# Kernel tuning notes

Measured on AMD Instinct MI355X. Metric: run time of the kernel, lower is better.

## Reference

```python
import jax, jax.numpy as jnp
import numpy as np

B, N, D, H = 32, 512, 768, 12
HD = D // H  # 64
EPS = 1e-5


def layer_norm(x, g, b):
    mu = jnp.mean(x, axis=-1, keepdims=True)
    var = jnp.mean((x - mu) ** 2, axis=-1, keepdims=True)
    return (x - mu) / jnp.sqrt(var + EPS) * g + b


def setup_inputs() -> dict:
    key = jax.random.key(0)
    ks = jax.random.split(key, 10)
    x = jax.random.normal(ks[0], (B, N, D), dtype=jnp.float32)
    adj = jax.random.randint(ks[1], (B, N, N), 0, 2).astype(jnp.int32)
    adj = jnp.maximum(adj, jnp.eye(N, dtype=jnp.int32)[None])  # self-loops
    init = lambda k, shape: (jax.random.normal(k, shape, dtype=jnp.float32) * 0.02)
    return {
        "x": x, "adj": adj,
        "wq": init(ks[2], (D, D)), "bq": jnp.zeros((D,), jnp.float32),
        "wk": init(ks[3], (D, D)), "bk": jnp.zeros((D,), jnp.float32),
        "wv": init(ks[4], (D, D)), "bv": jnp.zeros((D,), jnp.float32),
        "wo": init(ks[5], (D, D)), "bo": jnp.zeros((D,), jnp.float32),
        "g1": jnp.ones((D,), jnp.float32), "b1": jnp.zeros((D,), jnp.float32),
        "g2": jnp.ones((D,), jnp.float32), "b2": jnp.zeros((D,), jnp.float32),
        "w_ffn1": init(ks[6], (D, 4 * D)), "b_ffn1": jnp.zeros((4 * D,), jnp.float32),
        "w_ffn2": init(ks[7], (4 * D, D)), "b_ffn2": jnp.zeros((D,), jnp.float32),
    }


def reference(x, adj, wq, bq, wk, bk, wv, bv, wo, bo, g1, b1, g2, b2,
              w_ffn1, b_ffn1, w_ffn2, b_ffn2):
    scale = HD ** -0.5
    h = layer_norm(x, g1, b1)
    split = lambda t: t.reshape(B, N, H, HD).transpose(0, 2, 1, 3)  # [B,H,N,HD]
    q = split(h @ wq + bq)
    k = split(h @ wk + bk)
    v = split(h @ wv + bv)
    scores = jnp.einsum('bhnd,bhmd->bhnm', q, k) * scale  # [B,H,N,N]
    scores = jnp.where(adj[:, None, :, :] == 0, -jnp.inf, scores)
    attn = jax.nn.softmax(scores, axis=-1)
    attn = jnp.nan_to_num(attn, nan=0.0)  # rows with no edges -> 0
    out = jnp.einsum('bhnm,bhmd->bhnd', attn, v)
    out = out.transpose(0, 2, 1, 3).reshape(B, N, D)
    out = out @ wo + bo + x  # residual (dropout=0, eval mode)
    h2 = layer_norm(out, g2, b2)
    ffn = jax.nn.gelu(h2 @ w_ffn1 + b_ffn1, approximate=False) @ w_ffn2 + b_ffn2
    return out + ffn
```

## Files before the change

kernel.cpp:

```cpp
#include <hip/hip_runtime.h>


#define Bn 32
#define Nn 512
#define Dn 768
#define Hn 12
#define HDn 64
#define Mn (Bn * Nn)
#define DFn 3072
#define MCHUNK 8192

typedef unsigned short u16;
typedef unsigned long long u64;
typedef short bf16x8 __attribute__((ext_vector_type(8)));
typedef float f32x4 __attribute__((ext_vector_type(4)));
typedef unsigned short u16x8 __attribute__((ext_vector_type(8)));

__device__ __forceinline__ float b2f(u16 u) {
    return __uint_as_float(((unsigned int)u) << 16);
}
__device__ __forceinline__ u16 f2b(float f) {
    unsigned int u = __float_as_uint(f);
    u += 0x7fffu + ((u >> 16) & 1u);
    return (u16)(u >> 16);
}
__device__ __forceinline__ float loadDyn(const void* p, size_t i, int f) {
    return f ? ((const float*)p)[i] : b2f(((const u16*)p)[i]);
}
__device__ __forceinline__ float gelu_exact(float x) {
    return 0.5f * x * (1.0f + erff(x * 0.70710678118654752f));
}

__device__ __forceinline__ void gl_lds16(const u16* g, u16* l) {
    __builtin_amdgcn_global_load_lds(
        (const __attribute__((address_space(1))) void*)(unsigned long long)(const void*)g,
        (__attribute__((address_space(3))) void*)(unsigned)(unsigned long long)(void*)l,
        16, 0, 0);
}

__global__ __launch_bounds__(256) void sniff_k(const u16* __restrict__ x,
                                               int* __restrict__ flag) {
    const int idx = blockIdx.x * 256 + threadIdx.x;
    u16x8 a = *(const u16x8*)&x[(size_t)idx * 8];
    int cnt = 0;
#pragma unroll
    for (int e = 0; e < 8; e++)
        cnt += ((a[e] & 0x7F80) == 0x7F80) ? 1 : 0;
#pragma unroll
    for (int off = 1; off <= 32; off <<= 1) cnt += __shfl_xor(cnt, off, 64);
    if ((threadIdx.x & 63) == 0 && cnt > 0) atomicAdd(flag, cnt);
}

__device__ __forceinline__ int flagval(const int* flagp) {
    return (*flagp > 32) ? 1 : 0;
}

__global__ __launch_bounds__(256) void pack_bias_k(
    const void* __restrict__ bq, const void* __restrict__ bk,
    const void* __restrict__ bv, const void* __restrict__ bo,
    const void* __restrict__ bf1, const void* __restrict__ bf2,
    float* __restrict__ out, const int* __restrict__ flagp) {
    const int f = flagval(flagp);
    const int i = blockIdx.x * 256 + threadIdx.x;
    if (i >= 6912) return;
    const void* src;
    int off;
    if (i < 768)       { src = bq;  off = i; }
    else if (i < 1536) { src = bk;  off = i - 768; }
    else if (i < 2304) { src = bv;  off = i - 1536; }
    else if (i < 3072) { src = bo;  off = i - 2304; }
    else if (i < 6144) { src = bf1; off = i - 3072; }
    else               { src = bf2; off = i - 6144; }
    out[i] = loadDyn(src, off, f);
}

__global__ __launch_bounds__(256) void mask_build_k(
    const int* __restrict__ adj, u64* __restrict__ mask) {
    const int idx = blockIdx.x * 256 + threadIdx.x;
    const size_t base = (size_t)(idx >> 3) * Nn + (size_t)(idx & 7) * 64;
    const int4* p = (const int4*)(adj + base);
    u64 m = 0;
#pragma unroll
    for (int c = 0; c < 16; c++) {
        int4 a = p[c];
        if (a.x) m |= 1ull << (c * 4 + 0);
        if (a.y) m |= 1ull << (c * 4 + 1);
        if (a.z) m |= 1ull << (c * 4 + 2);
        if (a.w) m |= 1ull << (c * 4 + 3);
    }
    mask[idx] = m;
}

__global__ __launch_bounds__(256) void transpose_k(
    const void* __restrict__ in, u16* __restrict__ out, int R, int C,
    const int* __restrict__ flagp) {
    const int f = flagval(flagp);
    __shared__ u16 tile[32][33];
    int c0 = blockIdx.x * 32, r0 = blockIdx.y * 32;
    int tx = threadIdx.x, ty = threadIdx.y;
#pragma unroll
    for (int i = 0; i < 32; i += 8)
        tile[ty + i][tx] = f2b(loadDyn(in, (size_t)(r0 + ty + i) * C + c0 + tx, f));
    __syncthreads();
#pragma unroll
    for (int i = 0; i < 32; i += 8)
        out[(size_t)(c0 + ty + i) * R + r0 + tx] = tile[tx][ty + i];
}

__global__ __launch_bounds__(256) void vtrans_k(
    const u16* __restrict__ v, u16* __restrict__ vt) {
    __shared__ u16 tile[32][33];
    const int bh = blockIdx.z;
    const int d0 = blockIdx.x * 32;
    const int n0 = blockIdx.y * 32;
    const int b = bh / Hn, h = bh % Hn;
    const int tx = threadIdx.x, ty = threadIdx.y;
#pragma unroll
    for (int i = 0; i < 32; i += 8)
        tile[ty + i][tx] =
            v[(size_t)(b * Nn + n0 + ty + i) * Dn + h * HDn + d0 + tx];
    __syncthreads();
#pragma unroll
    for (int i = 0; i < 32; i += 8)
        vt[((size_t)bh * HDn + d0 + ty + i) * Nn + n0 + tx] = tile[tx][ty + i];
}

template <int XDYN>
__global__ __launch_bounds__(256) void ln_k(
    const void* __restrict__ x, const void* __restrict__ g,
    const void* __restrict__ b, u16* __restrict__ y,
    const int* __restrict__ flagp) {
    const int f = flagval(flagp);
    const int t = threadIdx.x;
    const int row = blockIdx.x * 8 + (t >> 5);
    const int l32 = t & 31;
    const size_t base = (size_t)row * Dn;
    float v[24];
    if (XDYN == 0 || f == 0) {
        const u16* xp = (const u16*)x;
#pragma unroll
        for (int kk = 0; kk < 3; kk++) {
            u16x8 a = *(const u16x8*)&xp[base + kk * 256 + l32 * 8];
#pragma unroll
            for (int e = 0; e < 8; e++) v[kk * 8 + e] = b2f(a[e]);
        }
    } else {
#pragma unroll
        for (int kk = 0; kk < 3; kk++)
#pragma unroll
            for (int e = 0; e < 8; e++)
                v[kk * 8 + e] = loadDyn(x, base + kk * 256 + l32 * 8 + e, f);
    }
    float s = 0.f;
#pragma unroll
    for (int i = 0; i < 24; i++) s += v[i];
#pragma unroll
    for (int off = 1; off <= 16; off <<= 1) s += __shfl_xor(s, off, 64);
    const float mu = s * (1.0f / Dn);
    float d2 = 0.f;
#pragma unroll
    for (int i = 0; i < 24; i++) { float d = v[i] - mu; d2 += d * d; }
#pragma unroll
    for (int off = 1; off <= 16; off <<= 1) d2 += __shfl_xor(d2, off, 64);
    const float rstd = rsqrtf(d2 * (1.0f / Dn) + 1e-5f);
#pragma unroll
    for (int kk = 0; kk < 3; kk++) {
        const int c0 = kk * 256 + l32 * 8;
        u16x8 o;
        if (f == 0) {
            u16x8 gv = *(const u16x8*)&((const u16*)g)[c0];
            u16x8 bv = *(const u16x8*)&((const u16*)b)[c0];
#pragma unroll
            for (int e = 0; e < 8; e++)
                o[e] = f2b((v[kk * 8 + e] - mu) * rstd * b2f(gv[e]) + b2f(bv[e]));
        } else {
#pragma unroll
            for (int e = 0; e < 8; e++)
                o[e] = f2b((v[kk * 8 + e] - mu) * rstd * loadDyn(g, c0 + e, f)
                           + loadDyn(b, c0 + e, f));
        }
        *(u16x8*)&y[base + c0] = o;
    }
}

template <int ACT, int RES, int STORE, int WN, int CSPLIT>
__global__ __launch_bounds__(256, 3) void gemm_bt(
    const u16* __restrict__ A, const u16* __restrict__ Bt,
    const float* __restrict__ bias, const void* __restrict__ res,
    void* __restrict__ C, int M, int N, int K, int moff,
    const int* __restrict__ flagp) {
    constexpr int BN = 2 * WN;
    constexpr int NJ = WN / 16;
    constexpr int NB = BN / 64;
    const int f = flagval(flagp);
    __shared__ __align__(16) u16 As[2][128 * 32];
    __shared__ __align__(16) u16 Bs[2][BN * 32];
    const int tid = threadIdx.x;
    const int m0 = blockIdx.x * 128, n0 = blockIdx.y * BN;
    const int wave = tid >> 6, lane = tid & 63;
    const int wm = (wave & 1) * 64, wn = (wave >> 1) * WN;
    const int lm = lane & 15, quad = lane >> 4;

    const int koff = (tid & 3) * 8;
    const int srow = tid >> 2;
    const u16* gA[2];
    const u16* gB[NB];
#pragma unroll
    for (int i = 0; i < 2; i++)
        gA[i] = A + (size_t)(m0 + srow + i * 64) * K + koff;
#pragma unroll
    for (int i = 0; i < NB; i++)
        gB[i] = Bt + (size_t)(n0 + srow + i * 64) * K + koff;

    f32x4 acc[4][NJ] = {};

    auto stage = [&](int buf) {
#pragma unroll
        for (int i = 0; i < 2; i++) {
            gl_lds16(gA[i], &As[buf][(tid + i * 256) * 8]);
            gA[i] += 32;
        }
#pragma unroll
        for (int i = 0; i < NB; i++) {
            gl_lds16(gB[i], &Bs[buf][(tid + i * 256) * 8]);
            gB[i] += 32;
        }
    };
    auto compute = [&](int buf) {
        bf16x8 af[4], bfv[NJ];
#pragma unroll
        for (int i = 0; i < 4; i++)
            af[i] = *(const bf16x8*)&As[buf][(wm + i * 16 + lm) * 32 + quad * 8];
#pragma unroll
        for (int j = 0; j < NJ; j++)
            bfv[j] = *(const bf16x8*)&Bs[buf][(wn + j * 16 + lm) * 32 + quad * 8];
#pragma unroll
        for (int i = 0; i < 4; i++)
#pragma unroll
            for (int j = 0; j < NJ; j++)
                acc[i][j] = __builtin_amdgcn_mfma_f32_16x16x32_bf16(
                    af[i], bfv[j], acc[i][j], 0, 0, 0);
    };

    stage(0);
    int cur = 0;
    for (int k0 = 32; k0 < K; k0 += 32) {
        __syncthreads();
        stage(cur ^ 1);
        compute(cur);
        cur ^= 1;
    }
    __syncthreads();
    compute(cur);

    float bias_f[NJ];
#pragma unroll
    for (int j = 0; j < NJ; j++)
        bias_f[j] = bias[n0 + wn + j * 16 + lm];
#pragma unroll
    for (int i = 0; i < 4; i++) {
#pragma unroll
        for (int r = 0; r < 4; r++) {
            const int row = m0 + wm + i * 16 + quad * 4 + r;
#pragma unroll
            for (int j = 0; j < NJ; j++) {
                int col = n0 + wn + j * 16 + lm;
                size_t rb;
                if (CSPLIT > 0) {
                    const int reg = col / CSPLIT;
                    rb = ((size_t)reg * M + moff + row) * (size_t)CSPLIT;
                    col -= reg * CSPLIT;
                } else {
                    rb = (size_t)(moff + row) * N;
                }
                float vv = acc[i][j][r] + bias_f[j];
                if (ACT == 1) vv = gelu_exact(vv);
                if (RES == 1) vv += b2f(((const u16*)res)[rb + col]);
                if (RES == 2) vv += loadDyn(res, rb + col, f);
                if (STORE == 0) ((u16*)C)[rb + col] = f2b(vv);
                else {
                    if (f) ((float*)C)[rb + col] = vv;
                    else   ((u16*)C)[rb + col] = f2b(vv);
                }
            }
        }
    }
}

__global__ __launch_bounds__(256) void attn_mfma_k(
    const u16* q, const u16* __restrict__ k,
    const u16* __restrict__ vt, const u64* __restrict__ mask, u16* o) {
    const int h = blockIdx.x, qg = blockIdx.y, b = blockIdx.z;
    const int q0 = qg * 64;
    const int tid = threadIdx.x;
    const int wave = tid >> 6, lane = tid & 63;
    const int lm = lane & 15, quad = lane >> 4;
    const int wm = wave * 16;
    const int bh = b * Hn + h;

    __shared__ __align__(16) u16 Qs[64 * 72];
    __shared__ __align__(16) u16 Ks[64 * 72];
    __shared__ __align__(16) u16 Vts[64 * 72];
    __shared__ __align__(16) u16 Ps[64 * 72];

    {
        const int row = tid >> 2, dc = (tid & 3) * 16;
        const u16* src = q + ((size_t)(b * Nn + q0 + row)) * Dn + h * HDn + dc;
        *(u16x8*)&Qs[row * 72 + dc]     = *(const u16x8*)src;
        *(u16x8*)&Qs[row * 72 + dc + 8] = *(const u16x8*)(src + 8);
    }

    float m_i[4], l_i[4];
#pragma unroll
    for (int r = 0; r < 4; r++) { m_i[r] = -3e38f; l_i[r] = 0.f; }
    f32x4 Oacc[4] = {};

    for (int kb = 0; kb < Nn / 64; kb++) {
        const int kb0 = kb * 64;
        __syncthreads();
        {
            const int row = tid >> 2, dc = (tid & 3) * 16;
            const u16* ksrc = k + ((size_t)(b * Nn + kb0 + row)) * Dn + h * HDn + dc;
            *(u16x8*)&Ks[row * 72 + dc]     = *(const u16x8*)ksrc;
            *(u16x8*)&Ks[row * 72 + dc + 8] = *(const u16x8*)(ksrc + 8);
            const int dim = tid >> 2, ks = (tid & 3) * 16;
            const u16* vsrc = vt + ((size_t)bh * HDn + dim) * Nn + kb0 + ks;
            *(u16x8*)&Vts[dim * 72 + ks]     = *(const u16x8*)vsrc;
            *(u16x8*)&Vts[dim * 72 + ks + 8] = *(const u16x8*)(vsrc + 8);
        }
        __syncthreads();
        f32x4 sacc[4] = {};
#pragma unroll
        for (int s = 0; s < 2; s++) {
            bf16x8 aq = *(const bf16x8*)&Qs[(wm + lm) * 72 + s * 32 + quad * 8];
#pragma unroll
            for (int j = 0; j < 4; j++) {
                bf16x8 bk = *(const bf16x8*)&Ks[(j * 16 + lm) * 72 + s * 32 + quad * 8];
                sacc[j] = __builtin_amdgcn_mfma_f32_16x16x32_bf16(aq, bk, sacc[j], 0, 0, 0);
            }
        }
        float pmax[4];
#pragma unroll
        for (int r = 0; r < 4; r++) {
            const u64 mrow = mask[(size_t)(b * Nn + q0 + wm + quad * 4 + r) * 8 + kb];
            float mx = -3e38f;
#pragma unroll
            for (int j = 0; j < 4; j++) {
                const int bit = (int)((mrow >> (j * 16 + lm)) & 1ull);
                float sc = bit ? sacc[j][r] * 0.125f : -3e38f;
                sacc[j][r] = sc;
                mx = fmaxf(mx, sc);
            }
            mx = fmaxf(mx, __shfl_xor(mx, 1, 64));
            mx = fmaxf(mx, __shfl_xor(mx, 2, 64));
            mx = fmaxf(mx, __shfl_xor(mx, 4, 64));
            mx = fmaxf(mx, __shfl_xor(mx, 8, 64));
            pmax[r] = mx;
        }
        float alpha[4];
#pragma unroll
        for (int r = 0; r < 4; r++) {
            float newm = fmaxf(m_i[r], pmax[r]);
            alpha[r] = __expf(m_i[r] - newm);
            m_i[r] = newm;
            float s_ = 0.f;
#pragma unroll
            for (int j = 0; j < 4; j++) {
                float sc = sacc[j][r];
                float p = (sc > -1e30f) ? __expf(sc - newm) : 0.f;
                sacc[j][r] = p;
                s_ += p;
            }
            s_ += __shfl_xor(s_, 1, 64);
            s_ += __shfl_xor(s_, 2, 64);
            s_ += __shfl_xor(s_, 4, 64);
            s_ += __shfl_xor(s_, 8, 64);
            l_i[r] = l_i[r] * alpha[r] + s_;
        }
#pragma unroll
        for (int r = 0; r < 4; r++)
#pragma unroll
            for (int j = 0; j < 4; j++)
                Ps[(wm + quad * 4 + r) * 72 + j * 16 + lm] = f2b(sacc[j][r]);
#pragma unroll
        for (int j = 0; j < 4; j++)
#pragma unroll
            for (int r = 0; r < 4; r++) Oacc[j][r] *= alpha[r];
        __syncthreads();
#pragma unroll
        for (int s = 0; s < 2; s++) {
            bf16x8 ap = *(const bf16x8*)&Ps[(wm + lm) * 72 + s * 32 + quad * 8];
#pragma unroll
            for (int j = 0; j < 4; j++) {
                bf16x8 bv = *(const bf16x8*)&Vts[(j * 16 + lm) * 72 + s * 32 + quad * 8];
                Oacc[j] = __builtin_amdgcn_mfma_f32_16x16x32_bf16(ap, bv, Oacc[j], 0, 0, 0);
            }
        }
    }
    float inv[4];
#pragma unroll
    for (int r = 0; r < 4; r++) inv[r] = (l_i[r] > 0.f) ? 1.0f / l_i[r] : 0.f;
#pragma unroll
    for (int r = 0; r < 4; r++) {
        const int row = q0 + wm + quad * 4 + r;
        u16* dst = o + ((size_t)(b * Nn + row)) * Dn + h * HDn;
#pragma unroll
        for (int j = 0; j < 4; j++)
            dst[j * 16 + lm] = f2b(Oacc[j][r] * inv[r]);
    }
}

extern "C" void kernel_launch(void* const* d_in, const int* in_sizes, int n_in,
                              void* d_out, int out_size, void* d_ws,
                              size_t ws_size, hipStream_t stream) {
    const void* x   = d_in[0];
    const int* adj  = (const int*)d_in[1];
    const void* wq  = d_in[2];
    const void* bq  = d_in[3];
    const void* wk  = d_in[4];
    const void* bk  = d_in[5];
    const void* wv  = d_in[6];
    const void* bv  = d_in[7];
    const void* wo  = d_in[8];
    const void* bo  = d_in[9];
    const void* g1  = d_in[10];
    const void* b1  = d_in[11];
    const void* g2  = d_in[12];
    const void* b2  = d_in[13];
    const void* w1  = d_in[14];
    const void* bf1 = d_in[15];
    const void* w2  = d_in[16];
    const void* bf2 = d_in[17];

    char* ws = (char*)d_ws;
    size_t off = 0;
    auto alloc = [&](size_t bytes) -> char* {
        char* p = ws + off;
        off += (bytes + 255) & ~(size_t)255;
        return p;
    };
    int* flag = (int*)alloc(4);
    u16* wqkvT = (u16*)alloc((size_t)3 * Dn * Dn * 2);
    u16* woT  = (u16*)alloc((size_t)Dn * Dn * 2);
    u16* w1T  = (u16*)alloc((size_t)Dn * DFn * 2);
    u16* w2T  = (u16*)alloc((size_t)Dn * DFn * 2);
    float* biasf = (float*)alloc(6912 * 4);
    u64* maskbuf = (u64*)alloc((size_t)Mn * 8 * 8);
    const size_t S = (size_t)Mn * Dn * 2;
    u16* Rh = (u16*)alloc(S);
    u16* Rq = (u16*)alloc(S);
    u16* Rk = (u16*)alloc(S);
    u16* Rv = (u16*)alloc(S);

    hipMemsetAsync(flag, 0, 4, stream);
    sniff_k<<<64, 256, 0, stream>>>((const u16*)x, flag);
    mask_build_k<<<Mn * 8 / 256, 256, 0, stream>>>(adj, maskbuf);
    pack_bias_k<<<27, 256, 0, stream>>>(bq, bk, bv, bo, bf1, bf2, biasf, flag);

    dim3 tb(32, 8);
    transpose_k<<<dim3(Dn / 32, Dn / 32), tb, 0, stream>>>(wq, wqkvT, Dn, Dn, flag);
    transpose_k<<<dim3(Dn / 32, Dn / 32), tb, 0, stream>>>(wk, wqkvT + (size_t)Dn * Dn, Dn, Dn, flag);
    transpose_k<<<dim3(Dn / 32, Dn / 32), tb, 0, stream>>>(wv, wqkvT + (size_t)2 * Dn * Dn, Dn, Dn, flag);
    transpose_k<<<dim3(Dn / 32, Dn / 32), tb, 0, stream>>>(wo, woT, Dn, Dn, flag);
    transpose_k<<<dim3(DFn / 32, Dn / 32), tb, 0, stream>>>(w1, w1T, Dn, DFn, flag);
    transpose_k<<<dim3(Dn / 32, DFn / 32), tb, 0, stream>>>(w2, w2T, DFn, Dn, flag);

    ln_k<1><<<Mn / 8, 256, 0, stream>>>(x, g1, b1, Rh, flag);

    gemm_bt<0, 0, 0, 64, Dn><<<dim3(Mn / 128, 3 * Dn / 128), 256, 0, stream>>>(
        Rh, wqkvT, biasf, nullptr, Rq, Mn, 3 * Dn, Dn, 0, flag);

    vtrans_k<<<dim3(HDn / 32, Nn / 32, Bn * Hn), tb, 0, stream>>>(Rv, Rh);

    attn_mfma_k<<<dim3(Hn, Nn / 64, Bn), 256, 0, stream>>>(Rq, Rk, Rh, maskbuf, Rq);

    gemm_bt<0, 2, 0, 64, 0><<<dim3(Mn / 128, Dn / 128), 256, 0, stream>>>(
        Rq, woT, biasf + 2304, x, Rv, Mn, Dn, Dn, 0, flag);

    ln_k<0><<<Mn / 8, 256, 0, stream>>>(Rv, g2, b2, Rh, flag);

    u16* hidden = Rq;
    for (int c = 0; c < Mn / MCHUNK; c++) {
        gemm_bt<1, 0, 0, 64, 0><<<dim3(MCHUNK / 128, DFn / 128), 256, 0, stream>>>(
            Rh + (size_t)c * MCHUNK * Dn, w1T, biasf + 3072, nullptr, hidden,
            MCHUNK, DFn, Dn, 0, flag);
        gemm_bt<0, 1, 1, 64, 0><<<dim3(MCHUNK / 128, Dn / 128), 256, 0, stream>>>(
            hidden, w2T, biasf + 6144, Rv, d_out, MCHUNK, Dn, DFn, c * MCHUNK, flag);
    }
}
```

Before: 679.7 us.

## Prefetch K/V tiles into registers and streamline the attention softmax loop

```diff
diff --git a/kernel.cpp b/kernel.cpp
--- a/kernel.cpp
+++ b/kernel.cpp
@@ -297,85 +297,84 @@
     const int lm = lane & 15, quad = lane >> 4;
     const int wm = wave * 16;
     const int bh = b * Hn + h;
-
-    __shared__ __align__(16) u16 Qs[64 * 72];
+    const float SC2 = 0.125f * 1.4426950408889634f;
+
     __shared__ __align__(16) u16 Ks[64 * 72];
     __shared__ __align__(16) u16 Vts[64 * 72];
     __shared__ __align__(16) u16 Ps[64 * 72];
 
-    {
-        const int row = tid >> 2, dc = (tid & 3) * 16;
-        const u16* src = q + ((size_t)(b * Nn + q0 + row)) * Dn + h * HDn + dc;
-        *(u16x8*)&Qs[row * 72 + dc]     = *(const u16x8*)src;
-        *(u16x8*)&Qs[row * 72 + dc + 8] = *(const u16x8*)(src + 8);
-    }
-
-    float m_i[4], l_i[4];
-#pragma unroll
-    for (int r = 0; r < 4; r++) { m_i[r] = -3e38f; l_i[r] = 0.f; }
+    const u16* qrow = q + ((size_t)(b * Nn + q0 + wm + lm)) * Dn + h * HDn + quad * 8;
+    const bf16x8 aq0 = *(const bf16x8*)(qrow);
+    const bf16x8 aq1 = *(const bf16x8*)(qrow + 32);
+
+    const int srow = tid >> 2, scc = (tid & 3) * 16;
+    const u16* kbase = k + ((size_t)(b * Nn + srow)) * Dn + h * HDn + scc;
+    const u16* vbase = vt + ((size_t)bh * HDn + srow) * Nn + scc;
+
+    u16x8 kr0 = *(const u16x8*)(kbase);
+    u16x8 kr1 = *(const u16x8*)(kbase + 8);
+    u16x8 vr0 = *(const u16x8*)(vbase);
+    u16x8 vr1 = *(const u16x8*)(vbase + 8);
+
+    float m_i[4], l_p[4];
+#pragma unroll
+    for (int r = 0; r < 4; r++) { m_i[r] = -3e38f; l_p[r] = 0.f; }
     f32x4 Oacc[4] = {};
 
     for (int kb = 0; kb < Nn / 64; kb++) {
-        const int kb0 = kb * 64;
         __syncthreads();
-        {
-            const int row = tid >> 2, dc = (tid & 3) * 16;
-            const u16* ksrc = k + ((size_t)(b * Nn + kb0 + row)) * Dn + h * HDn + dc;
-            *(u16x8*)&Ks[row * 72 + dc]     = *(const u16x8*)ksrc;
-            *(u16x8*)&Ks[row * 72 + dc + 8] = *(const u16x8*)(ksrc + 8);
-            const int dim = tid >> 2, ks = (tid & 3) * 16;
-            const u16* vsrc = vt + ((size_t)bh * HDn + dim) * Nn + kb0 + ks;
-            *(u16x8*)&Vts[dim * 72 + ks]     = *(const u16x8*)vsrc;
-            *(u16x8*)&Vts[dim * 72 + ks + 8] = *(const u16x8*)(vsrc + 8);
-        }
+        *(u16x8*)&Ks[srow * 72 + scc]      = kr0;
+        *(u16x8*)&Ks[srow * 72 + scc + 8]  = kr1;
+        *(u16x8*)&Vts[srow * 72 + scc]     = vr0;
+        *(u16x8*)&Vts[srow * 72 + scc + 8] = vr1;
         __syncthreads();
+        if (kb + 1 < Nn / 64) {
+            const u16* kn = kbase + (size_t)(kb + 1) * 64 * Dn;
+            const u16* vn = vbase + (kb + 1) * 64;
+            kr0 = *(const u16x8*)(kn);
+            kr1 = *(const u16x8*)(kn + 8);
+            vr0 = *(const u16x8*)(vn);
+            vr1 = *(const u16x8*)(vn + 8);
+        }
         f32x4 sacc[4] = {};
+        __builtin_amdgcn_s_setprio(1);
 #pragma unroll
         for (int s = 0; s < 2; s++) {
-            bf16x8 aq = *(const bf16x8*)&Qs[(wm + lm) * 72 + s * 32 + quad * 8];
+            const bf16x8 aq = s == 0 ? aq0 : aq1;
 #pragma unroll
             for (int j = 0; j < 4; j++) {
                 bf16x8 bk = *(const bf16x8*)&Ks[(j * 16 + lm) * 72 + s * 32 + quad * 8];
                 sacc[j] = __builtin_amdgcn_mfma_f32_16x16x32_bf16(aq, bk, sacc[j], 0, 0, 0);
             }
         }
-        float pmax[4];
+        __builtin_amdgcn_s_setprio(0);
+        float alpha[4];
 #pragma unroll
         for (int r = 0; r < 4; r++) {
             const u64 mrow = mask[(size_t)(b * Nn + q0 + wm + quad * 4 + r) * 8 + kb];
-            float mx = -3e38f;
 #pragma unroll
             for (int j = 0; j < 4; j++) {
                 const int bit = (int)((mrow >> (j * 16 + lm)) & 1ull);
-                float sc = bit ? sacc[j][r] * 0.125f : -3e38f;
-                sacc[j][r] = sc;
-                mx = fmaxf(mx, sc);
+                sacc[j][r] = bit ? sacc[j][r] * SC2 : -3e38f;
             }
+            float mx = fmaxf(fmaxf(sacc[0][r], sacc[1][r]),
+                             fmaxf(sacc[2][r], sacc[3][r]));
             mx = fmaxf(mx, __shfl_xor(mx, 1, 64));
             mx = fmaxf(mx, __shfl_xor(mx, 2, 64));
             mx = fmaxf(mx, __shfl_xor(mx, 4, 64));
             mx = fmaxf(mx, __shfl_xor(mx, 8, 64));
-            pmax[r] = mx;
-        }
-        float alpha[4];
-#pragma unroll
-        for (int r = 0; r < 4; r++) {
-            float newm = fmaxf(m_i[r], pmax[r]);
-            alpha[r] = __expf(m_i[r] - newm);
+            const float newm = fmaxf(m_i[r], mx);
+            alpha[r] = exp2f(m_i[r] - newm);
             m_i[r] = newm;
             float s_ = 0.f;
 #pragma unroll
             for (int j = 0; j < 4; j++) {
-                float sc = sacc[j][r];
-                float p = (sc > -1e30f) ? __expf(sc - newm) : 0.f;
+                const float sc = sacc[j][r];
+                const float p = (sc > -1e30f) ? exp2f(sc - newm) : 0.f;
                 sacc[j][r] = p;
                 s_ += p;
             }
-            s_ += __shfl_xor(s_, 1, 64);
-            s_ += __shfl_xor(s_, 2, 64);
-            s_ += __shfl_xor(s_, 4, 64);
-            s_ += __shfl_xor(s_, 8, 64);
-            l_i[r] = l_i[r] * alpha[r] + s_;
+            l_p[r] = l_p[r] * alpha[r] + s_;
         }
 #pragma unroll
         for (int r = 0; r < 4; r++)
@@ -386,7 +385,7 @@
         for (int j = 0; j < 4; j++)
 #pragma unroll
             for (int r = 0; r < 4; r++) Oacc[j][r] *= alpha[r];
-        __syncthreads();
+        __builtin_amdgcn_s_setprio(1);
 #pragma unroll
         for (int s = 0; s < 2; s++) {
             bf16x8 ap = *(const bf16x8*)&Ps[(wm + lm) * 72 + s * 32 + quad * 8];
@@ -396,10 +395,18 @@
                 Oacc[j] = __builtin_amdgcn_mfma_f32_16x16x32_bf16(ap, bv, Oacc[j], 0, 0, 0);
             }
         }
+        __builtin_amdgcn_s_setprio(0);
     }
     float inv[4];
 #pragma unroll
-    for (int r = 0; r < 4; r++) inv[r] = (l_i[r] > 0.f) ? 1.0f / l_i[r] : 0.f;
+    for (int r = 0; r < 4; r++) {
+        float l = l_p[r];
+        l += __shfl_xor(l, 1, 64);
+        l += __shfl_xor(l, 2, 64);
+        l += __shfl_xor(l, 4, 64);
+        l += __shfl_xor(l, 8, 64);
+        inv[r] = (l > 0.f) ? 1.0f / l : 0.f;
+    }
 #pragma unroll
     for (int r = 0; r < 4; r++) {
         const int row = q0 + wm + quad * 4 + r;
```

Measured after the change: 689.4 us. About the same (+1.4%).
